# Kernel tuning notes

Measured on AMD Instinct MI355X. Metric: run time of the kernel, lower is better.

## Reference

```python
import jax, jax.numpy as jnp
import numpy as np
from jax import lax

B, T, D, H = 32, 2048, 128, 256

def _lstm_dir(x, w_ih, w_hh, b_ih, b_hh, h0, c0, reverse):
    # x: (B,T,Din). Precompute input contributions for all timesteps.
    xw = jnp.einsum('btd,gd->tbg', x, w_ih) + (b_ih + b_hh)  # (T,B,4H)
    def step(carry, xt):
        h, c = carry
        g = xt + h @ w_hh.T                      # (B,4H), gate order i,f,g,o
        i, f, gg, o = jnp.split(g, 4, axis=-1)
        c = jax.nn.sigmoid(f) * c + jax.nn.sigmoid(i) * jnp.tanh(gg)
        h = jax.nn.sigmoid(o) * jnp.tanh(c)
        return (h, c), h
    (hn, cn), hs = lax.scan(step, (h0, c0), xw, reverse=reverse)
    return hs.transpose(1, 0, 2), hn, cn          # (B,T,H), (B,H), (B,H)

def _bilstm(x, pf, pr, h0f, c0f, h0r, c0r):
    of, hnf, cnf = _lstm_dir(x, *pf, h0f, c0f, False)
    orv, hnr, cnr = _lstm_dir(x, *pr, h0r, c0r, True)
    return jnp.concatenate([of, orv], axis=-1), hnf, cnf, hnr, cnr

def setup_inputs() -> dict:
    key = jax.random.key(0)
    ks = jax.random.split(key, 20)
    s = 0.05
    d = {'x': jax.random.normal(ks[0], (B, T, D), jnp.float32)}
    def mk(k, shape):
        return jax.random.normal(k, shape, jnp.float32) * s
    # layer 1 (input D), forward and reverse directions
    d['w_ih1_f'] = mk(ks[1], (4*H, D)); d['w_hh1_f'] = mk(ks[2], (4*H, H))
    d['b_ih1_f'] = mk(ks[3], (4*H,));  d['b_hh1_f'] = mk(ks[4], (4*H,))
    d['w_ih1_r'] = mk(ks[5], (4*H, D)); d['w_hh1_r'] = mk(ks[6], (4*H, H))
    d['b_ih1_r'] = mk(ks[7], (4*H,));  d['b_hh1_r'] = mk(ks[8], (4*H,))
    # layer 2 (input 2H)
    d['w_ih2_f'] = mk(ks[9], (4*H, 2*H)); d['w_hh2_f'] = mk(ks[10], (4*H, H))
    d['b_ih2_f'] = mk(ks[11], (4*H,));   d['b_hh2_f'] = mk(ks[12], (4*H,))
    d['w_ih2_r'] = mk(ks[13], (4*H, 2*H)); d['w_hh2_r'] = mk(ks[14], (4*H, H))
    d['b_ih2_r'] = mk(ks[15], (4*H,));    d['b_hh2_r'] = mk(ks[16], (4*H,))
    d['fc_w'] = mk(ks[17], (1, 2*H)); d['fc_b'] = mk(ks[18], (1,))
    return d

def reference(x, w_ih1_f, w_hh1_f, b_ih1_f, b_hh1_f,
              w_ih1_r, w_hh1_r, b_ih1_r, b_hh1_r,
              w_ih2_f, w_hh2_f, b_ih2_f, b_hh2_f,
              w_ih2_r, w_hh2_r, b_ih2_r, b_hh2_r,
              fc_w, fc_b):
    z = jnp.zeros((x.shape[0], H), x.dtype)
    # layer 1, zero initial state
    out1, hnf, cnf, hnr, cnr = _bilstm(
        x, (w_ih1_f, w_hh1_f, b_ih1_f, b_hh1_f),
        (w_ih1_r, w_hh1_r, b_ih1_r, b_hh1_r), z, z, z, z)
    # layer 2 initialized with layer 1 final (h,c) per direction (as in the
    # original: lstm2(lstm_out, lstm_c))
    out2, _, _, _, _ = _bilstm(
        out1, (w_ih2_f, w_hh2_f, b_ih2_f, b_hh2_f),
        (w_ih2_r, w_hh2_r, b_ih2_r, b_hh2_r), hnf, cnf, hnr, cnr)
    y = jnp.tanh(out2 @ fc_w.T + fc_b)            # (B,T,1)
    return y.reshape(y.shape[0], -1)[:, None, :]  # (B,1,T)
```

## Files before the change

kernel.cpp:

```cpp
#include <hip/hip_runtime.h>

#define BB 32
#define TT 2048
#define DD 128
#define HH 256
#define NTH 512
#define NRANK 32
#define NGRP 8
#define HASHK 2654435761u

typedef float f32x4 __attribute__((ext_vector_type(4)));
typedef unsigned int u32;
typedef u32 u32x2 __attribute__((ext_vector_type(2)));
typedef u32 u32x4 __attribute__((ext_vector_type(4)));

__device__ __forceinline__ float sigm(float x)  { return 1.0f / (1.0f + __expf(-x)); }
__device__ __forceinline__ float tanh_f(float x){ return 1.0f - 2.0f / (__expf(2.0f * x) + 1.0f); }

template<int KIN, int LAYER>
__global__ __launch_bounds__(NTH, 1)
void lstm_scan(const float* __restrict__ in_seq, long sb, long st,
               const float* __restrict__ wih_f, const float* __restrict__ whh_f,
               const float* __restrict__ bih_f, const float* __restrict__ bhh_f,
               const float* __restrict__ wih_r, const float* __restrict__ whh_r,
               const float* __restrict__ bih_r, const float* __restrict__ bhh_r,
               float* __restrict__ hseed,
               float* __restrict__ cseed,
               u32* __restrict__ hbt,
               float* __restrict__ out1,
               float* __restrict__ acc,
               const float* __restrict__ fcw,
               int never)
{
    constexpr int KINP = KIN + 4;
    constexpr int HHP  = HH + 4;
    constexpr int C4   = KIN / 4;
    constexpr int XC   = KIN / 128;
    constexpr int NPXI = (8 * C4 + NTH - 1) / NTH;
    constexpr int RSTR = 36;
    constexpr int PADN = (LAYER == 1) ? 8192 : 5120;

    const int blk  = blockIdx.x;
    const int g    = blk & 7;
    const int rank = blk >> 3;
    const int dir  = g & 1;
    const int bq   = g >> 1;
    const int tid  = threadIdx.x;

    __shared__ __align__(16) float zx[8][KINP];
    __shared__ __align__(16) float zh[8][HHP];
    __shared__ __align__(16) float red2[256 * RSTR];
    __shared__ float gates_s[4][8][9];
    __shared__ float bias_s[32];
    __shared__ float padlds[PADN];
    if (never) padlds[never & (PADN - 1)] = 1.0f;

    const float* wih = dir ? wih_r : wih_f;
    const float* whh = dir ? whh_r : whh_f;
    const float* bih = dir ? bih_r : bih_f;
    const float* bhh = dir ? bhh_r : bhh_f;

    const int bh = tid >> 8;
    const int rg = (tid >> 5) & 7;
    const int sl = tid & 31;

    f32x4 wx[4][XC], wh[4][2];
    #pragma unroll
    for (int rr = 0; rr < 4; ++rr) {
        const int r = rg * 4 + rr;
        const int grow = (r >> 3) * HH + rank * 8 + (r & 7);
        #pragma unroll
        for (int c = 0; c < XC; ++c)
            wx[rr][c] = *(const f32x4*)(wih + (long)grow * KIN + sl * 4 + 128 * c);
        #pragma unroll
        for (int c = 0; c < 2; ++c)
            wh[rr][c] = *(const f32x4*)(whh + (long)grow * HH + sl * 4 + 128 * c);
    }
    if (tid < 32) {
        const int grow = (tid >> 3) * HH + rank * 8 + (tid & 7);
        bias_s[tid] = bih[grow] + bhh[grow];
    }

    u32* hbt_g = hbt + g * (2 * 256 * 8 * 2);
    float* hs_seed = hseed + g * (8 * HH);
    float* cs_seed = cseed + g * (8 * HH);

    const int jj2   = tid >> 3;
    const int bl2   = tid & 7;
    const int jglob = rank * 8 + jj2;

    float creg = 0.0f, fcv = 0.0f;
    if (tid < 64 && LAYER == 2) {
        creg = cs_seed[bl2 * HH + jglob];
        fcv  = fcw[dir * HH + jglob];
    }

    {
        const int t0 = dir ? (TT - 1) : 0;
        const long tb = (long)t0 * st;
        for (int q = tid; q < 8 * C4; q += NTH) {
            const int bl = q / C4;
            const int k4 = q - bl * C4;
            *(f32x4*)&zx[bl][k4 * 4] =
                *(const f32x4*)(in_seq + (long)(bq * 8 + bl) * sb + tb + k4 * 4);
        }
        if (tid < 64) {
            const float h0 = (LAYER == 1) ? 0.0f : hs_seed[bl2 * HH + jglob];
            const u32 hx = __float_as_uint(h0);
            u32x2 pkt; pkt.x = hx; pkt.y = 1u + hx * HASHK;
            u32* pp = hbt_g + ((0 * 256 + jglob) * 8 + bl2) * 2;
            asm volatile("global_store_dwordx2 %0, %1, off sc0 sc1"
                         :: "v"(pp), "v"(pkt) : "memory");
        }
    }
    __syncthreads();

    for (int s = 0; s < TT; ++s) {
        const int t = dir ? (TT - 1 - s) : s;

        f32x4 px[NPXI];
        if (s + 1 < TT) {
            const long tb = (long)(dir ? (t - 1) : (t + 1)) * st;
            #pragma unroll
            for (int i = 0; i < NPXI; ++i) {
                const int q = tid + i * NTH;
                if (q < 8 * C4) {
                    const int bl = q / C4;
                    const int k4 = q - bl * C4;
                    px[i] = *(const f32x4*)(in_seq + (long)(bq * 8 + bl) * sb + tb + k4 * 4);
                }
            }
        }

        float ac[4][4];
        #pragma unroll
        for (int rr = 0; rr < 4; ++rr)
            #pragma unroll
            for (int b = 0; b < 4; ++b) ac[rr][b] = 0.0f;
        #pragma unroll
        for (int c = 0; c < XC; ++c) {
            f32x4 zv[4];
            #pragma unroll
            for (int b = 0; b < 4; ++b)
                zv[b] = *(const f32x4*)&zx[bh * 4 + b][sl * 4 + 128 * c];
            #pragma unroll
            for (int rr = 0; rr < 4; ++rr) {
                const f32x4 w = wx[rr][c];
                #pragma unroll
                for (int b = 0; b < 4; ++b)
                    ac[rr][b] = fmaf(w.x, zv[b].x, fmaf(w.y, zv[b].y,
                                fmaf(w.z, zv[b].z, fmaf(w.w, zv[b].w, ac[rr][b]))));
            }
        }

        if (tid < 256) {
            const u32 tg = (u32)(s + 1);
            const u32* hp = hbt_g + (((s & 1) * 256 + tid) * 8) * 2;
            u32x4 q0, q1, q2, q3;
            while (true) {
                asm volatile(
                    "global_load_dwordx4 %0, %4, off sc0 sc1\n\t"
                    "global_load_dwordx4 %1, %4, off offset:16 sc0 sc1\n\t"
                    "global_load_dwordx4 %2, %4, off offset:32 sc0 sc1\n\t"
                    "global_load_dwordx4 %3, %4, off offset:48 sc0 sc1\n\t"
                    "s_waitcnt vmcnt(0)"
                    : "=&v"(q0), "=&v"(q1), "=&v"(q2), "=&v"(q3)
                    : "v"(hp) : "memory");
                const bool ok =
                    (q0.y - q0.x * HASHK == tg) && (q0.w - q0.z * HASHK == tg) &&
                    (q1.y - q1.x * HASHK == tg) && (q1.w - q1.z * HASHK == tg) &&
                    (q2.y - q2.x * HASHK == tg) && (q2.w - q2.z * HASHK == tg) &&
                    (q3.y - q3.x * HASHK == tg) && (q3.w - q3.z * HASHK == tg);
                if (ok) break;
                __builtin_amdgcn_s_sleep(1);
            }
            zh[0][tid] = __uint_as_float(q0.x);
            zh[1][tid] = __uint_as_float(q0.z);
            zh[2][tid] = __uint_as_float(q1.x);
            zh[3][tid] = __uint_as_float(q1.z);
            zh[4][tid] = __uint_as_float(q2.x);
            zh[5][tid] = __uint_as_float(q2.z);
            zh[6][tid] = __uint_as_float(q3.x);
            zh[7][tid] = __uint_as_float(q3.z);
        }
        __syncthreads();

        #pragma unroll
        for (int c = 0; c < 2; ++c) {
            f32x4 zv[4];
            #pragma unroll
            for (int b = 0; b < 4; ++b)
                zv[b] = *(const f32x4*)&zh[bh * 4 + b][sl * 4 + 128 * c];
            #pragma unroll
            for (int rr = 0; rr < 4; ++rr) {
                const f32x4 w = wh[rr][c];
                #pragma unroll
                for (int b = 0; b < 4; ++b)
                    ac[rr][b] = fmaf(w.x, zv[b].x, fmaf(w.y, zv[b].y,
                                fmaf(w.z, zv[b].z, fmaf(w.w, zv[b].w, ac[rr][b]))));
            }
        }
        #pragma unroll
        for (int rr = 0; rr < 4; ++rr)
            #pragma unroll
            for (int b = 0; b < 4; ++b)
                red2[((rg * 4 + rr) * 8 + bh * 4 + b) * RSTR + sl] = ac[rr][b];
        __syncthreads();

        if (tid < 256) {
            float sg = bias_s[tid >> 3];
            const f32x4* rp = (const f32x4*)&red2[tid * RSTR];
            #pragma unroll
            for (int q = 0; q < 8; ++q) {
                const f32x4 v = rp[q];
                sg += v.x + v.y + v.z + v.w;
            }
            gates_s[tid >> 6][(tid >> 3) & 7][tid & 7] = sg;
        }
        __syncthreads();

        if (tid < 64) {
            const float gi = gates_s[0][jj2][bl2];
            const float gf = gates_s[1][jj2][bl2];
            const float gg = gates_s[2][jj2][bl2];
            const float go = gates_s[3][jj2][bl2];
            creg = sigm(gf) * creg + sigm(gi) * tanh_f(gg);
            const float hv = sigm(go) * tanh_f(creg);
            if (s + 1 < TT) {
                const u32 hx = __float_as_uint(hv);
                u32x2 pkt; pkt.x = hx; pkt.y = (u32)(s + 2) + hx * HASHK;
                u32* pp = hbt_g + ((((s + 1) & 1) * 256 + jglob) * 8 + bl2) * 2;
                asm volatile("global_store_dwordx2 %0, %1, off sc0 sc1"
                             :: "v"(pp), "v"(pkt) : "memory");
            }
            if (LAYER == 1) {
                out1[(long)t * (BB * 2 * HH) + (bq * 8 + bl2) * (2 * HH) + dir * HH + jglob] = hv;
                if (s == TT - 1) {
                    hs_seed[bl2 * HH + jglob] = hv;
                    cs_seed[bl2 * HH + jglob] = creg;
                }
            } else {
                float val = hv * fcv;
                val += __shfl_down(val, 32, 64);
                val += __shfl_down(val, 16, 64);
                val += __shfl_down(val, 8, 64);
                if (jj2 == 0) atomicAdd(&acc[t * BB + bq * 8 + bl2], val);
            }
        }
        if (s + 1 < TT) {
            #pragma unroll
            for (int i = 0; i < NPXI; ++i) {
                const int q = tid + i * NTH;
                if (q < 8 * C4) {
                    const int bl = q / C4;
                    const int k4 = q - bl * C4;
                    *(f32x4*)&zx[bl][k4 * 4] = px[i];
                }
            }
        }
        __syncthreads();
    }
}

__global__ void finalize_k(const float* __restrict__ acc, const float* __restrict__ fcb,
                           float* __restrict__ out)
{
    const int i = blockIdx.x * blockDim.x + threadIdx.x;
    if (i < BB * TT) {
        const int b = i >> 11;
        const int t = i & (TT - 1);
        out[i] = tanhf(acc[t * BB + b] + fcb[0]);
    }
}

extern "C" void kernel_launch(void* const* d_in, const int* in_sizes, int n_in,
                              void* d_out, int out_size, void* d_ws, size_t ws_size,
                              hipStream_t stream) {
    const float* x     = (const float*)d_in[0];
    const float* wih1f = (const float*)d_in[1];
    const float* whh1f = (const float*)d_in[2];
    const float* bih1f = (const float*)d_in[3];
    const float* bhh1f = (const float*)d_in[4];
    const float* wih1r = (const float*)d_in[5];
    const float* whh1r = (const float*)d_in[6];
    const float* bih1r = (const float*)d_in[7];
    const float* bhh1r = (const float*)d_in[8];
    const float* wih2f = (const float*)d_in[9];
    const float* whh2f = (const float*)d_in[10];
    const float* bih2f = (const float*)d_in[11];
    const float* bhh2f = (const float*)d_in[12];
    const float* wih2r = (const float*)d_in[13];
    const float* whh2r = (const float*)d_in[14];
    const float* bih2r = (const float*)d_in[15];
    const float* bhh2r = (const float*)d_in[16];
    const float* fcw   = (const float*)d_in[17];
    const float* fcb   = (const float*)d_in[18];

    char* ws = (char*)d_ws;
    size_t off = 0;
    float* acc  = (float*)(ws + off); off += (size_t)TT * BB * 4;
    u32* hbt1   = (u32*)(ws + off);   off += (size_t)NGRP * 2 * 256 * 8 * 2 * 4;
    u32* hbt2   = (u32*)(ws + off);   off += (size_t)NGRP * 2 * 256 * 8 * 2 * 4;
    float* hseed = (float*)(ws + off); off += (size_t)NGRP * 8 * HH * 4;
    float* cseed = (float*)(ws + off); off += (size_t)NGRP * 8 * HH * 4;
    const size_t clear_bytes = off;
    float* out1 = (float*)(ws + off); off += (size_t)TT * BB * 2 * HH * 4;

    hipMemsetAsync(d_ws, 0, clear_bytes, stream);

    lstm_scan<DD, 1><<<NGRP * NRANK, NTH, 0, stream>>>(
        x, (long)TT * DD, (long)DD,
        wih1f, whh1f, bih1f, bhh1f, wih1r, whh1r, bih1r, bhh1r,
        hseed, cseed, hbt1, out1, nullptr, nullptr, 0);

    lstm_scan<2 * HH, 2><<<NGRP * NRANK, NTH, 0, stream>>>(
        out1, (long)(2 * HH), (long)(BB * 2 * HH),
        wih2f, whh2f, bih2f, bhh2f, wih2r, whh2r, bih2r, bhh2r,
        hseed, cseed, hbt2, nullptr, acc, fcw, 0);

    finalize_k<<<(BB * TT + 255) / 256, 256, 0, stream>>>(acc, fcb, (float*)d_out);
}
```

Measured before the change: 10.40 ms.

## Keep per-step inputs in registers and overlap h-spin loads with x prefetch

Removes the shared-memory staging buffer for the input timestep. Each thread now loads its own slice of x straight into registers for the next step. The first spin-poll loads of the hidden-state exchange are issued before the x prefetch, and a partial vmcnt wait lets the poll complete without waiting on the prefetch, so the two memory latencies overlap. The end-of-step __syncthreads is dropped, shortening the serial recurrence per step. The cost is more VGPRs for layer 2, redundant global loads of x across warps, and reliance on other barriers for zh safety.

```diff
diff --git a/kernel.cpp b/kernel.cpp
--- a/kernel.cpp
+++ b/kernel.cpp
@@ -16,6 +16,16 @@
 
 __device__ __forceinline__ float sigm(float x)  { return 1.0f / (1.0f + __expf(-x)); }
 __device__ __forceinline__ float tanh_f(float x){ return 1.0f - 2.0f / (__expf(2.0f * x) + 1.0f); }
+
+#define SPIN_ISSUE asm volatile( \
+    "global_load_dwordx4 %0, %4, off sc0 sc1\n\t" \
+    "global_load_dwordx4 %1, %4, off offset:16 sc0 sc1\n\t" \
+    "global_load_dwordx4 %2, %4, off offset:32 sc0 sc1\n\t" \
+    "global_load_dwordx4 %3, %4, off offset:48 sc0 sc1" \
+    : "=&v"(q0), "=&v"(q1), "=&v"(q2), "=&v"(q3) : "v"(hp) : "memory")
+
+#define WAIT_TIED(N) asm volatile("s_waitcnt vmcnt(" #N ")" \
+    : "+v"(q0), "+v"(q1), "+v"(q2), "+v"(q3) :: "memory")
 
 template<int KIN, int LAYER>
 __global__ __launch_bounds__(NTH, 1)
@@ -32,13 +42,10 @@
                const float* __restrict__ fcw,
                int never)
 {
-    constexpr int KINP = KIN + 4;
     constexpr int HHP  = HH + 4;
-    constexpr int C4   = KIN / 4;
     constexpr int XC   = KIN / 128;
-    constexpr int NPXI = (8 * C4 + NTH - 1) / NTH;
     constexpr int RSTR = 36;
-    constexpr int PADN = (LAYER == 1) ? 8192 : 5120;
+    constexpr int PADN = 9216;
 
     const int blk  = blockIdx.x;
     const int g    = blk & 7;
@@ -47,7 +54,6 @@
     const int bq   = g >> 1;
     const int tid  = threadIdx.x;
 
-    __shared__ __align__(16) float zx[8][KINP];
     __shared__ __align__(16) float zh[8][HHP];
     __shared__ __align__(16) float red2[256 * RSTR];
     __shared__ float gates_s[4][8][9];
@@ -95,15 +101,16 @@
         fcv  = fcw[dir * HH + jglob];
     }
 
+    f32x4 xr[4][XC];
     {
         const int t0 = dir ? (TT - 1) : 0;
         const long tb = (long)t0 * st;
-        for (int q = tid; q < 8 * C4; q += NTH) {
-            const int bl = q / C4;
-            const int k4 = q - bl * C4;
-            *(f32x4*)&zx[bl][k4 * 4] =
-                *(const f32x4*)(in_seq + (long)(bq * 8 + bl) * sb + tb + k4 * 4);
-        }
+        #pragma unroll
+        for (int bi = 0; bi < 4; ++bi)
+            #pragma unroll
+            for (int c = 0; c < XC; ++c)
+                xr[bi][c] = *(const f32x4*)(in_seq +
+                    (long)(bq * 8 + bh * 4 + bi) * sb + tb + sl * 4 + 128 * c);
         if (tid < 64) {
             const float h0 = (LAYER == 1) ? 0.0f : hs_seed[bl2 * HH + jglob];
             const u32 hx = __float_as_uint(h0);
@@ -118,20 +125,6 @@
     for (int s = 0; s < TT; ++s) {
         const int t = dir ? (TT - 1 - s) : s;
 
-        f32x4 px[NPXI];
-        if (s + 1 < TT) {
-            const long tb = (long)(dir ? (t - 1) : (t + 1)) * st;
-            #pragma unroll
-            for (int i = 0; i < NPXI; ++i) {
-                const int q = tid + i * NTH;
-                if (q < 8 * C4) {
-                    const int bl = q / C4;
-                    const int k4 = q - bl * C4;
-                    px[i] = *(const f32x4*)(in_seq + (long)(bq * 8 + bl) * sb + tb + k4 * 4);
-                }
-            }
-        }
-
         float ac[4][4];
         #pragma unroll
         for (int rr = 0; rr < 4; ++rr)
@@ -139,33 +132,38 @@
             for (int b = 0; b < 4; ++b) ac[rr][b] = 0.0f;
         #pragma unroll
         for (int c = 0; c < XC; ++c) {
-            f32x4 zv[4];
-            #pragma unroll
-            for (int b = 0; b < 4; ++b)
-                zv[b] = *(const f32x4*)&zx[bh * 4 + b][sl * 4 + 128 * c];
             #pragma unroll
             for (int rr = 0; rr < 4; ++rr) {
                 const f32x4 w = wx[rr][c];
                 #pragma unroll
-                for (int b = 0; b < 4; ++b)
-                    ac[rr][b] = fmaf(w.x, zv[b].x, fmaf(w.y, zv[b].y,
-                                fmaf(w.z, zv[b].z, fmaf(w.w, zv[b].w, ac[rr][b]))));
-            }
-        }
-
+                for (int b = 0; b < 4; ++b) {
+                    const f32x4 zv = xr[b][c];
+                    ac[rr][b] = fmaf(w.x, zv.x, fmaf(w.y, zv.y,
+                                fmaf(w.z, zv.z, fmaf(w.w, zv.w, ac[rr][b]))));
+                }
+            }
+        }
+
+        const u32 tg = (u32)(s + 1);
+        const u32* hp = hbt_g + (((s & 1) * 256 + tid) * 8) * 2;
+        u32x4 q0, q1, q2, q3;
+        if (tid < 256) { SPIN_ISSUE; }
+        if (s + 1 < TT) {
+            const long tb = (long)(dir ? (t - 1) : (t + 1)) * st;
+            #pragma unroll
+            for (int bi = 0; bi < 4; ++bi)
+                #pragma unroll
+                for (int c = 0; c < XC; ++c)
+                    xr[bi][c] = *(const f32x4*)(in_seq +
+                        (long)(bq * 8 + bh * 4 + bi) * sb + tb + sl * 4 + 128 * c);
+        }
         if (tid < 256) {
-            const u32 tg = (u32)(s + 1);
-            const u32* hp = hbt_g + (((s & 1) * 256 + tid) * 8) * 2;
-            u32x4 q0, q1, q2, q3;
+            if (s + 1 < TT) {
+                if constexpr (XC == 1) { WAIT_TIED(4); } else { WAIT_TIED(16); }
+            } else {
+                WAIT_TIED(0);
+            }
             while (true) {
-                asm volatile(
-                    "global_load_dwordx4 %0, %4, off sc0 sc1\n\t"
-                    "global_load_dwordx4 %1, %4, off offset:16 sc0 sc1\n\t"
-                    "global_load_dwordx4 %2, %4, off offset:32 sc0 sc1\n\t"
-                    "global_load_dwordx4 %3, %4, off offset:48 sc0 sc1\n\t"
-                    "s_waitcnt vmcnt(0)"
-                    : "=&v"(q0), "=&v"(q1), "=&v"(q2), "=&v"(q3)
-                    : "v"(hp) : "memory");
                 const bool ok =
                     (q0.y - q0.x * HASHK == tg) && (q0.w - q0.z * HASHK == tg) &&
                     (q1.y - q1.x * HASHK == tg) && (q1.w - q1.z * HASHK == tg) &&
@@ -173,6 +171,8 @@
                     (q3.y - q3.x * HASHK == tg) && (q3.w - q3.z * HASHK == tg);
                 if (ok) break;
                 __builtin_amdgcn_s_sleep(1);
+                SPIN_ISSUE;
+                WAIT_TIED(0);
             }
             zh[0][tid] = __uint_as_float(q0.x);
             zh[1][tid] = __uint_as_float(q0.z);
@@ -247,18 +247,6 @@
                 if (jj2 == 0) atomicAdd(&acc[t * BB + bq * 8 + bl2], val);
             }
         }
-        if (s + 1 < TT) {
-            #pragma unroll
-            for (int i = 0; i < NPXI; ++i) {
-                const int q = tid + i * NTH;
-                if (q < 8 * C4) {
-                    const int bl = q / C4;
-                    const int k4 = q - bl * C4;
-                    *(f32x4*)&zx[bl][k4 * 4] = px[i];
-                }
-            }
-        }
-        __syncthreads();
     }
 }
 
```

Result: slower. 18.01 ms (+73.1%).

## Use fp16 packed dot products for LSTM gate matvecs and drop a barrier

Applied to the files above, without the earlier changes.

Weights and the staged input/hidden vectors are converted to fp16 and the gate accumulation uses packed fdot2 instructions with fp32 accumulation, which halves the FMA-type instruction count and the LDS traffic per step. The store of the next step's input into shared memory moves before an earlier barrier, so the trailing per-step __syncthreads is removed. This lowers precision on a 2048-step recurrence, which risks accumulated error. The LDS padding sizes are adjusted to match the smaller buffers.

```diff
diff --git a/kernel.cpp b/kernel.cpp
--- a/kernel.cpp
+++ b/kernel.cpp
@@ -13,6 +13,18 @@
 typedef unsigned int u32;
 typedef u32 u32x2 __attribute__((ext_vector_type(2)));
 typedef u32 u32x4 __attribute__((ext_vector_type(4)));
+typedef _Float16 f16;
+typedef f16 f16x2 __attribute__((ext_vector_type(2)));
+typedef f16 f16x4 __attribute__((ext_vector_type(4)));
+
+#if defined(__has_builtin)
+#if __has_builtin(__builtin_amdgcn_fdot2)
+#define FDOT2(a, b, c) __builtin_amdgcn_fdot2((a), (b), (c), false)
+#endif
+#endif
+#ifndef FDOT2
+#define FDOT2(a, b, c) ((c) + (float)(a)[0] * (float)(b)[0] + (float)(a)[1] * (float)(b)[1])
+#endif
 
 __device__ __forceinline__ float sigm(float x)  { return 1.0f / (1.0f + __expf(-x)); }
 __device__ __forceinline__ float tanh_f(float x){ return 1.0f - 2.0f / (__expf(2.0f * x) + 1.0f); }
@@ -38,7 +50,7 @@
     constexpr int XC   = KIN / 128;
     constexpr int NPXI = (8 * C4 + NTH - 1) / NTH;
     constexpr int RSTR = 36;
-    constexpr int PADN = (LAYER == 1) ? 8192 : 5120;
+    constexpr int PADN = (LAYER == 1) ? 9600 : 8192;
 
     const int blk  = blockIdx.x;
     const int g    = blk & 7;
@@ -47,8 +59,8 @@
     const int bq   = g >> 1;
     const int tid  = threadIdx.x;
 
-    __shared__ __align__(16) float zx[8][KINP];
-    __shared__ __align__(16) float zh[8][HHP];
+    __shared__ __align__(16) f16 zx[8][KINP];
+    __shared__ __align__(16) f16 zh[8][HHP];
     __shared__ __align__(16) float red2[256 * RSTR];
     __shared__ float gates_s[4][8][9];
     __shared__ float bias_s[32];
@@ -64,17 +76,27 @@
     const int rg = (tid >> 5) & 7;
     const int sl = tid & 31;
 
-    f32x4 wx[4][XC], wh[4][2];
+    f16x2 wxp[4][XC][2], whp[4][2][2];
     #pragma unroll
     for (int rr = 0; rr < 4; ++rr) {
         const int r = rg * 4 + rr;
         const int grow = (r >> 3) * HH + rank * 8 + (r & 7);
         #pragma unroll
-        for (int c = 0; c < XC; ++c)
-            wx[rr][c] = *(const f32x4*)(wih + (long)grow * KIN + sl * 4 + 128 * c);
-        #pragma unroll
-        for (int c = 0; c < 2; ++c)
-            wh[rr][c] = *(const f32x4*)(whh + (long)grow * HH + sl * 4 + 128 * c);
+        for (int c = 0; c < XC; ++c) {
+            const f32x4 wv = *(const f32x4*)(wih + (long)grow * KIN + sl * 4 + 128 * c);
+            f16x2 lo, hi;
+            lo[0] = (f16)wv.x; lo[1] = (f16)wv.y;
+            hi[0] = (f16)wv.z; hi[1] = (f16)wv.w;
+            wxp[rr][c][0] = lo; wxp[rr][c][1] = hi;
+        }
+        #pragma unroll
+        for (int c = 0; c < 2; ++c) {
+            const f32x4 wv = *(const f32x4*)(whh + (long)grow * HH + sl * 4 + 128 * c);
+            f16x2 lo, hi;
+            lo[0] = (f16)wv.x; lo[1] = (f16)wv.y;
+            hi[0] = (f16)wv.z; hi[1] = (f16)wv.w;
+            whp[rr][c][0] = lo; whp[rr][c][1] = hi;
+        }
     }
     if (tid < 32) {
         const int grow = (tid >> 3) * HH + rank * 8 + (tid & 7);
@@ -101,8 +123,10 @@
         for (int q = tid; q < 8 * C4; q += NTH) {
             const int bl = q / C4;
             const int k4 = q - bl * C4;
-            *(f32x4*)&zx[bl][k4 * 4] =
-                *(const f32x4*)(in_seq + (long)(bq * 8 + bl) * sb + tb + k4 * 4);
+            const f32x4 v = *(const f32x4*)(in_seq + (long)(bq * 8 + bl) * sb + tb + k4 * 4);
+            f16x4 h4;
+            h4[0] = (f16)v.x; h4[1] = (f16)v.y; h4[2] = (f16)v.z; h4[3] = (f16)v.w;
+            *(f16x4*)&zx[bl][k4 * 4] = h4;
         }
         if (tid < 64) {
             const float h0 = (LAYER == 1) ? 0.0f : hs_seed[bl2 * HH + jglob];
@@ -139,18 +163,20 @@
             for (int b = 0; b < 4; ++b) ac[rr][b] = 0.0f;
         #pragma unroll
         for (int c = 0; c < XC; ++c) {
-            f32x4 zv[4];
-            #pragma unroll
-            for (int b = 0; b < 4; ++b)
-                zv[b] = *(const f32x4*)&zx[bh * 4 + b][sl * 4 + 128 * c];
-            #pragma unroll
-            for (int rr = 0; rr < 4; ++rr) {
-                const f32x4 w = wx[rr][c];
+            f16x2 zlo[4], zhi[4];
+            #pragma unroll
+            for (int b = 0; b < 4; ++b) {
+                const f16x4 zv = *(const f16x4*)&zx[bh * 4 + b][sl * 4 + 128 * c];
+                zlo[b] = __builtin_shufflevector(zv, zv, 0, 1);
+                zhi[b] = __builtin_shufflevector(zv, zv, 2, 3);
+            }
+            #pragma unroll
+            for (int rr = 0; rr < 4; ++rr)
                 #pragma unroll
-                for (int b = 0; b < 4; ++b)
-                    ac[rr][b] = fmaf(w.x, zv[b].x, fmaf(w.y, zv[b].y,
-                                fmaf(w.z, zv[b].z, fmaf(w.w, zv[b].w, ac[rr][b]))));
-            }
+                for (int b = 0; b < 4; ++b) {
+                    ac[rr][b] = FDOT2(wxp[rr][c][0], zlo[b], ac[rr][b]);
+                    ac[rr][b] = FDOT2(wxp[rr][c][1], zhi[b], ac[rr][b]);
+                }
         }
 
         if (tid < 256) {
@@ -174,37 +200,53 @@
                 if (ok) break;
                 __builtin_amdgcn_s_sleep(1);
             }
-            zh[0][tid] = __uint_as_float(q0.x);
-            zh[1][tid] = __uint_as_float(q0.z);
-            zh[2][tid] = __uint_as_float(q1.x);
-            zh[3][tid] = __uint_as_float(q1.z);
-            zh[4][tid] = __uint_as_float(q2.x);
-            zh[5][tid] = __uint_as_float(q2.z);
-            zh[6][tid] = __uint_as_float(q3.x);
-            zh[7][tid] = __uint_as_float(q3.z);
+            zh[0][tid] = (f16)__uint_as_float(q0.x);
+            zh[1][tid] = (f16)__uint_as_float(q0.z);
+            zh[2][tid] = (f16)__uint_as_float(q1.x);
+            zh[3][tid] = (f16)__uint_as_float(q1.z);
+            zh[4][tid] = (f16)__uint_as_float(q2.x);
+            zh[5][tid] = (f16)__uint_as_float(q2.z);
+            zh[6][tid] = (f16)__uint_as_float(q3.x);
+            zh[7][tid] = (f16)__uint_as_float(q3.z);
         }
         __syncthreads();
 
         #pragma unroll
         for (int c = 0; c < 2; ++c) {
-            f32x4 zv[4];
-            #pragma unroll
-            for (int b = 0; b < 4; ++b)
-                zv[b] = *(const f32x4*)&zh[bh * 4 + b][sl * 4 + 128 * c];
-            #pragma unroll
-            for (int rr = 0; rr < 4; ++rr) {
-                const f32x4 w = wh[rr][c];
+            f16x2 zlo[4], zhi[4];
+            #pragma unroll
+            for (int b = 0; b < 4; ++b) {
+                const f16x4 zv = *(const f16x4*)&zh[bh * 4 + b][sl * 4 + 128 * c];
+                zlo[b] = __builtin_shufflevector(zv, zv, 0, 1);
+                zhi[b] = __builtin_shufflevector(zv, zv, 2, 3);
+            }
+            #pragma unroll
+            for (int rr = 0; rr < 4; ++rr)
                 #pragma unroll
-                for (int b = 0; b < 4; ++b)
-                    ac[rr][b] = fmaf(w.x, zv[b].x, fmaf(w.y, zv[b].y,
-                                fmaf(w.z, zv[b].z, fmaf(w.w, zv[b].w, ac[rr][b]))));
-            }
+                for (int b = 0; b < 4; ++b) {
+                    ac[rr][b] = FDOT2(whp[rr][c][0], zlo[b], ac[rr][b]);
+                    ac[rr][b] = FDOT2(whp[rr][c][1], zhi[b], ac[rr][b]);
+                }
         }
         #pragma unroll
         for (int rr = 0; rr < 4; ++rr)
             #pragma unroll
             for (int b = 0; b < 4; ++b)
                 red2[((rg * 4 + rr) * 8 + bh * 4 + b) * RSTR + sl] = ac[rr][b];
+        if (s + 1 < TT) {
+            #pragma unroll
+            for (int i = 0; i < NPXI; ++i) {
+                const int q = tid + i * NTH;
+                if (q < 8 * C4) {
+                    const int bl = q / C4;
+                    const int k4 = q - bl * C4;
+                    f16x4 h4;
+                    h4[0] = (f16)px[i].x; h4[1] = (f16)px[i].y;
+                    h4[2] = (f16)px[i].z; h4[3] = (f16)px[i].w;
+                    *(f16x4*)&zx[bl][k4 * 4] = h4;
+                }
+            }
+        }
         __syncthreads();
 
         if (tid < 256) {
@@ -247,18 +289,6 @@
                 if (jj2 == 0) atomicAdd(&acc[t * BB + bq * 8 + bl2], val);
             }
         }
-        if (s + 1 < TT) {
-            #pragma unroll
-            for (int i = 0; i < NPXI; ++i) {
-                const int q = tid + i * NTH;
-                if (q < 8 * C4) {
-                    const int bl = q / C4;
-                    const int k4 = q - bl * C4;
-                    *(f32x4*)&zx[bl][k4 * 4] = px[i];
-                }
-            }
-        }
-        __syncthreads();
     }
 }
 
```

Result: slower. 13.02 ms (+25.2%).
